# Kernel optimization log

Hardware: AMD Instinct MI355X
Metric: run time of the kernel (lower is better)

Reference implementation:

```python
import jax, jax.numpy as jnp
import numpy as np

N_ATOMS = 100000
N_PAIRS = 3200000
N_PROP = 16
N_BASIS = 10
W = 16  # MLP width for pp/pi/ii nodes


def setup_inputs() -> dict:
    key = jax.random.key(0)
    ks = jax.random.split(key, 16)
    s = 0.1
    inp = {
        "ind_2": jax.random.randint(ks[0], (N_PAIRS, 2), 0, N_ATOMS),
        "p1": jax.random.normal(ks[1], (N_ATOMS, N_PROP), dtype=jnp.float32),
        "basis": jax.random.normal(ks[2], (N_PAIRS, N_BASIS), dtype=jnp.float32),
        # pp_pre: [16,16], bias=True
        "Wpre0": jax.random.normal(ks[3], (N_PROP, W), dtype=jnp.float32) * s,
        "bpre0": jnp.zeros((W,), dtype=jnp.float32),
        "Wpre1": jax.random.normal(ks[4], (W, W), dtype=jnp.float32) * s,
        "bpre1": jnp.zeros((W,), dtype=jnp.float32),
        # pi: input 2*W -> W -> W*n_basis, bias=True
        "Wpi0": jax.random.normal(ks[5], (2 * W, W), dtype=jnp.float32) * s,
        "bpi0": jnp.zeros((W,), dtype=jnp.float32),
        "Wpi1": jax.random.normal(ks[6], (W, W * N_BASIS), dtype=jnp.float32) * s,
        "bpi1": jnp.zeros((W * N_BASIS,), dtype=jnp.float32),
        # ii: [16,16], bias=False
        "Wii0": jax.random.normal(ks[7], (W, W), dtype=jnp.float32) * s,
        "Wii1": jax.random.normal(ks[8], (W, W), dtype=jnp.float32) * s,
        # pp_post: [16,16], bias=False
        "Wpost0": jax.random.normal(ks[9], (W, W), dtype=jnp.float32) * s,
        "Wpost1": jax.random.normal(ks[10], (W, W), dtype=jnp.float32) * s,
    }
    return inp


def reference(ind_2, p1, basis, Wpre0, bpre0, Wpre1, bpre1,
              Wpi0, bpi0, Wpi1, bpi1, Wii0, Wii1, Wpost0, Wpost1):
    act = jnp.tanh
    n_atoms = p1.shape[0]
    # pp_pre: per-atom FF (activation on every dense, bias=True)
    p1_in = act(p1 @ Wpre0 + bpre0)
    p1_in = act(p1_in @ Wpre1 + bpre1)
    # PI: gather pair endpoints, concat, MLP, contract with radial basis
    h = jnp.concatenate([p1_in[ind_2[:, 0]], p1_in[ind_2[:, 1]]], axis=-1)  # (P, 2W)
    h = act(h @ Wpi0 + bpi0)                                                # (P, W)
    h = act(h @ Wpi1 + bpi1)                                                # (P, W*n_basis)
    h = h.reshape(h.shape[0], -1, basis.shape[-1])                          # (P, W, n_basis)
    i_pair = jnp.einsum('pcb,pb->pc', h, basis)                             # (P, W)
    # II: pair-mixing FF (bias=False)
    i_pair = act(i_pair @ Wii0)
    i_pair = act(i_pair @ Wii1)
    # IP: scatter-sum pair features back to atoms at ind_2[:,0]
    p_sum = jax.ops.segment_sum(i_pair, ind_2[:, 0], num_segments=n_atoms)  # (A, W)
    # pp_post (bias=False)
    p1_new = act(p_sum @ Wpost0)
    p1_new = act(p1_new @ Wpost1)
    return (p1_new, i_pair)
```

## Files before the change

kernel.cpp:

```cpp
#include <hip/hip_runtime.h>

#define N_ATOMS 100000
#define N_PAIRS 3200000
#define N_PROP 16
#define N_BASIS 10
#define W 16
#define NSUP (N_PAIRS / 32)
#define SCAN_BLK 1024
#define NB ((N_ATOMS + SCAN_BLK - 1) / SCAN_BLK)
#define SC 2.88539008177792681f

typedef short  s16x8  __attribute__((ext_vector_type(8)));
typedef float  f32x4  __attribute__((ext_vector_type(4)));
typedef float  f32x16 __attribute__((ext_vector_type(16)));

__device__ __forceinline__ float tanh_pre(float y) {
    float e = __builtin_amdgcn_exp2f(y);
    return 1.0f - 2.0f * __builtin_amdgcn_rcpf(e + 1.0f);
}
__device__ __forceinline__ float fast_tanh(float x) {
    float e = __builtin_amdgcn_exp2f(x * SC);
    return 1.0f - 2.0f * __builtin_amdgcn_rcpf(e + 1.0f);
}
__device__ __forceinline__ unsigned short bf16r(float f) {
    union { float f; unsigned u; } v; v.f = f;
    unsigned r = v.u + 0x7FFFu + ((v.u >> 16) & 1u);
    return (unsigned short)(r >> 16);
}
__device__ __forceinline__ unsigned cvt_pk_bf16(float a, float b) {
    unsigned r;
    asm("v_cvt_pk_bf16_f32 %0, %1, %2" : "=v"(r) : "v"(a), "v"(b));
    return r;
}
__device__ __forceinline__ float bitf(unsigned u) {
    union { unsigned u; float f; } v; v.u = u; return v.f;
}

__global__ __launch_bounds__(256) void k_pp_pre(
    const float* __restrict__ p1,
    const float* __restrict__ W0, const float* __restrict__ b0,
    const float* __restrict__ W1, const float* __restrict__ b1,
    const float* __restrict__ Wpi0, const float* __restrict__ bpi0,
    float* __restrict__ ytop, float* __restrict__ ybot)
{
    int a = blockIdx.x * 256 + threadIdx.x;
    if (a >= N_ATOMS) return;
    const float4* src = reinterpret_cast<const float4*>(p1 + (size_t)a * N_PROP);
    float4 v0 = src[0], v1 = src[1], v2 = src[2], v3 = src[3];
    float x[N_PROP] = {v0.x,v0.y,v0.z,v0.w, v1.x,v1.y,v1.z,v1.w,
                       v2.x,v2.y,v2.z,v2.w, v3.x,v3.y,v3.z,v3.w};
    float h[W];
#pragma unroll
    for (int c = 0; c < W; ++c) h[c] = b0[c];
#pragma unroll
    for (int k = 0; k < N_PROP; ++k)
#pragma unroll
        for (int c = 0; c < W; ++c) h[c] += x[k] * W0[k*W + c];
#pragma unroll
    for (int c = 0; c < W; ++c) h[c] = fast_tanh(h[c]);
    float y[W];
#pragma unroll
    for (int c = 0; c < W; ++c) y[c] = b1[c];
#pragma unroll
    for (int k = 0; k < W; ++k)
#pragma unroll
        for (int c = 0; c < W; ++c) y[c] += h[k] * W1[k*W + c];
    float t[W];
#pragma unroll
    for (int c = 0; c < W; ++c) t[c] = fast_tanh(y[c]);

    float yt[W], yb[W];
#pragma unroll
    for (int c = 0; c < W; ++c) { yt[c] = bpi0[c]; yb[c] = 0.0f; }
#pragma unroll
    for (int k = 0; k < W; ++k)
#pragma unroll
        for (int c = 0; c < W; ++c) {
            yt[c] += t[k] * Wpi0[k*W + c];
            yb[c] += t[k] * Wpi0[(W + k)*W + c];
        }
    float4* dt = reinterpret_cast<float4*>(ytop + (size_t)a * W);
    float4* db = reinterpret_cast<float4*>(ybot + (size_t)a * W);
#pragma unroll
    for (int q = 0; q < 4; ++q) {
        dt[q] = make_float4(SC*yt[4*q], SC*yt[4*q+1], SC*yt[4*q+2], SC*yt[4*q+3]);
        db[q] = make_float4(SC*yb[4*q], SC*yb[4*q+1], SC*yb[4*q+2], SC*yb[4*q+3]);
    }
}

template<int USE_RANK>
__global__ __launch_bounds__(256) void k_pair_mfma(
    const int*   __restrict__ ind2,
    const float* __restrict__ basis,
    const float* __restrict__ ytop,
    const float* __restrict__ ybot,
    const float* __restrict__ Wpi1, const float* __restrict__ bpi1,
    const float* __restrict__ Wii0, const float* __restrict__ Wii1,
    float* __restrict__ i_pair_out,
    const unsigned* __restrict__ starts,
    const unsigned* __restrict__ rank,
    unsigned* __restrict__ cursor,
    float* __restrict__ svals)
{
    __shared__ s16x8 aw_lds[5][2][32];
    __shared__ s16x8 ab_lds[5][2][32];

    const int lane = threadIdx.x & 63;
    const int wv   = threadIdx.x >> 6;
    const int col  = lane & 31;
    const int h    = lane >> 5;

    for (int e = threadIdx.x; e < 320; e += 256) {
        int T = e >> 6, hh = (e >> 5) & 1, row = e & 31;
        int colW = (4*(row >> 3) + (row & 3)) * N_BASIS + 2*T + ((row >> 2) & 1);
        s16x8 wfrag, bfrag;
#pragma unroll
        for (int j = 0; j < 8; ++j) {
            int k = 8*hh + j;
            wfrag[j] = (short)bf16r(SC * Wpi1[k*(W*N_BASIS) + colW]);
            bfrag[j] = (short)((k == 0) ? bf16r(SC * bpi1[colW]) : 0);
        }
        aw_lds[T][hh][row] = wfrag;
        ab_lds[T][hh][row] = bfrag;
    }

    s16x8 a3, a4;
#pragma unroll
    for (int j = 0; j < 8; ++j) {
        int k = 8*h + j;
        a3[j] = (short)(col < W ? bf16r(SC * Wii0[k*W + col]) : 0);
        a4[j] = (short)(col < W ? bf16r(SC * Wii1[k*W + col]) : 0);
    }
    s16x8 Bones = {0,0,0,0,0,0,0,0};
    if (h == 0) Bones[0] = (short)0x3F80;

    __syncthreads();

    const int stride = gridDim.x * 4;
    int sup = blockIdx.x * 4 + wv;
    if (sup >= NSUP) return;
    const int2* ind2v = reinterpret_cast<const int2*>(ind2);

    int2 ij = ind2v[(size_t)sup * 32 + col];
    f32x4 yt0 = *reinterpret_cast<const f32x4*>(ytop + (size_t)ij.x * W + 8*h);
    f32x4 yt1 = *reinterpret_cast<const f32x4*>(ytop + (size_t)ij.x * W + 8*h + 4);
    f32x4 yb0 = *reinterpret_cast<const f32x4*>(ybot + (size_t)ij.y * W + 8*h);
    f32x4 yb1 = *reinterpret_cast<const f32x4*>(ybot + (size_t)ij.y * W + 8*h + 4);

    for (; sup < NSUP; sup += stride) {
        const int p0 = sup * 32;
        const int p  = p0 + col;
        const int nsup = (sup + stride < NSUP) ? (sup + stride) : sup;

        int2 nij = ind2v[(size_t)nsup * 32 + col];

        float h0[8];
#pragma unroll
        for (int j = 0; j < 4; ++j) h0[j]     = tanh_pre(yt0[j] + yb0[j]);
#pragma unroll
        for (int j = 0; j < 4; ++j) h0[4 + j] = tanh_pre(yt1[j] + yb1[j]);
        unsigned w0h = cvt_pk_bf16(h0[0], h0[1]);
        unsigned w1h = cvt_pk_bf16(h0[2], h0[3]);
        unsigned w2h = cvt_pk_bf16(h0[4], h0[5]);
        unsigned w3h = cvt_pk_bf16(h0[6], h0[7]);
        unsigned w0l = cvt_pk_bf16(h0[0] - bitf(w0h << 16), h0[1] - bitf(w0h & 0xFFFF0000u));
        unsigned w1l = cvt_pk_bf16(h0[2] - bitf(w1h << 16), h0[3] - bitf(w1h & 0xFFFF0000u));
        unsigned w2l = cvt_pk_bf16(h0[4] - bitf(w2h << 16), h0[5] - bitf(w2h & 0xFFFF0000u));
        unsigned w3l = cvt_pk_bf16(h0[6] - bitf(w3h << 16), h0[7] - bitf(w3h & 0xFFFF0000u));
        union { unsigned u[4]; s16x8 v; } BH, BL;
        BH.u[0] = w0h; BH.u[1] = w1h; BH.u[2] = w2h; BH.u[3] = w3h;
        BL.u[0] = w0l; BL.u[1] = w1l; BL.u[2] = w2l; BL.u[3] = w3l;
        s16x8 B2h = BH.v, B2l = BL.v;

        const float2* bb = reinterpret_cast<const float2*>(basis + (size_t)p * N_BASIS);
        float bsel[5];
#pragma unroll
        for (int q = 0; q < 5; ++q) {
            float2 t2 = bb[q];
            bsel[q] = h ? t2.y : t2.x;
        }

        float v[16];
#pragma unroll
        for (int i = 0; i < 16; ++i) v[i] = 0.0f;
#pragma unroll
        for (int T = 0; T < 5; ++T) {
            s16x8 af = aw_lds[T][h][col];
            s16x8 ab = ab_lds[T][h][col];
            f32x16 z = {0.0f};
            z = __builtin_amdgcn_mfma_f32_32x32x16_bf16(ab, Bones, z, 0, 0, 0);
            z = __builtin_amdgcn_mfma_f32_32x32x16_bf16(af, B2h,  z, 0, 0, 0);
            z = __builtin_amdgcn_mfma_f32_32x32x16_bf16(af, B2l,  z, 0, 0, 0);
#pragma unroll
            for (int i = 0; i < 16; ++i)
                v[i] += tanh_pre(z[i]) * bsel[T];
        }

        f32x4 nyt0 = *reinterpret_cast<const f32x4*>(ytop + (size_t)nij.x * W + 8*h);
        f32x4 nyt1 = *reinterpret_cast<const f32x4*>(ytop + (size_t)nij.x * W + 8*h + 4);
        f32x4 nyb0 = *reinterpret_cast<const f32x4*>(ybot + (size_t)nij.y * W + 8*h);
        f32x4 nyb1 = *reinterpret_cast<const f32x4*>(ybot + (size_t)nij.y * W + 8*h + 4);

        float own[8], snd[8];
        if (h == 0) {
#pragma unroll
            for (int j = 0; j < 8; ++j) { own[j] = v[j]; snd[j] = v[8 + j]; }
        } else {
#pragma unroll
            for (int j = 0; j < 8; ++j) { own[j] = v[8 + j]; snd[j] = v[j]; }
        }
        float vf[8];
#pragma unroll
        for (int j = 0; j < 8; ++j) vf[j] = own[j] + __shfl_xor(snd[j], 32);

        union { unsigned u[4]; s16x8 v; } B3u;
        B3u.u[0] = cvt_pk_bf16(vf[0], vf[1]);
        B3u.u[1] = cvt_pk_bf16(vf[2], vf[3]);
        B3u.u[2] = cvt_pk_bf16(vf[4], vf[5]);
        B3u.u[3] = cvt_pk_bf16(vf[6], vf[7]);
        f32x16 ua = {0.0f};
        ua = __builtin_amdgcn_mfma_f32_32x32x16_bf16(a3, B3u.v, ua, 0, 0, 0);
        float u[8];
#pragma unroll
        for (int i = 0; i < 8; ++i) u[i] = tanh_pre(ua[i]);

        float uo[4], us[4];
        if (h == 0) {
#pragma unroll
            for (int j = 0; j < 4; ++j) { uo[j] = u[j]; us[j] = u[4 + j]; }
        } else {
#pragma unroll
            for (int j = 0; j < 4; ++j) { uo[j] = u[4 + j]; us[j] = u[j]; }
        }
        float ur[4];
#pragma unroll
        for (int j = 0; j < 4; ++j) ur[j] = __shfl_xor(us[j], 32);
        union { unsigned u[4]; s16x8 v; } B4u;
        if (h == 0) {
            B4u.u[0] = cvt_pk_bf16(uo[0], uo[1]);
            B4u.u[1] = cvt_pk_bf16(uo[2], uo[3]);
            B4u.u[2] = cvt_pk_bf16(ur[0], ur[1]);
            B4u.u[3] = cvt_pk_bf16(ur[2], ur[3]);
        } else {
            B4u.u[0] = cvt_pk_bf16(ur[0], ur[1]);
            B4u.u[1] = cvt_pk_bf16(ur[2], ur[3]);
            B4u.u[2] = cvt_pk_bf16(uo[0], uo[1]);
            B4u.u[3] = cvt_pk_bf16(uo[2], uo[3]);
        }
        f32x16 wa = {0.0f};
        wa = __builtin_amdgcn_mfma_f32_32x32x16_bf16(a4, B4u.v, wa, 0, 0, 0);
        float wq[8];
#pragma unroll
        for (int i = 0; i < 8; ++i) wq[i] = tanh_pre(wa[i]);

        unsigned pos;
        if (USE_RANK) {
            pos = starts[ij.x] + rank[p];
        } else {
            unsigned pp = 0;
            if (h == 0) pp = atomicAdd(&cursor[ij.x], 1u);
            pos = (unsigned)__shfl((int)pp, col);
        }

        const int rk0 = lane & 15;
        const int q   = lane >> 4;
#pragma unroll
        for (int k = 0; k < 2; ++k) {
            int row = 16*k + rk0;
            int src = row + 32*(q & 1);
            float vA0 = __shfl(wq[0], src), vA1 = __shfl(wq[1], src);
            float vA2 = __shfl(wq[2], src), vA3 = __shfl(wq[3], src);
            float vB0 = __shfl(wq[4], src), vB1 = __shfl(wq[5], src);
            float vB2 = __shfl(wq[6], src), vB3 = __shfl(wq[7], src);
            bool hiq = (q >= 2);
            f32x4 val = { hiq ? vB0 : vA0, hiq ? vB1 : vA1,
                          hiq ? vB2 : vA2, hiq ? vB3 : vA3 };
            unsigned posr = (unsigned)__shfl((int)pos, row);
            __builtin_nontemporal_store(val,
                reinterpret_cast<f32x4*>(i_pair_out + (size_t)(p0 + row) * W + q*4));
            __builtin_nontemporal_store(val,
                reinterpret_cast<f32x4*>(svals + (size_t)posr * W + q*4));
        }

        ij = nij;
        yt0 = nyt0; yt1 = nyt1; yb0 = nyb0; yb1 = nyb1;
    }
}

__global__ __launch_bounds__(256) void k_count(const int* __restrict__ ind2,
                                               unsigned* __restrict__ counts,
                                               unsigned* __restrict__ rank)
{
    int t = blockIdx.x * 256 + threadIdx.x;
    if (t >= N_PAIRS / 2) return;
    int4 ii = reinterpret_cast<const int4*>(ind2)[t];
    unsigned r0 = atomicAdd(&counts[ii.x], 1u);
    unsigned r1 = atomicAdd(&counts[ii.z], 1u);
    uint2 rr; rr.x = r0; rr.y = r1;
    *reinterpret_cast<uint2*>(rank + 2*t) = rr;
}

__global__ __launch_bounds__(SCAN_BLK) void k_scanA(const unsigned* __restrict__ counts,
                                                    unsigned* __restrict__ starts,
                                                    unsigned* __restrict__ bsum)
{
    __shared__ unsigned sc[SCAN_BLK];
    int a = blockIdx.x * SCAN_BLK + threadIdx.x;
    unsigned c = (a < N_ATOMS) ? counts[a] : 0u;
    sc[threadIdx.x] = c;
    __syncthreads();
    for (int off = 1; off < SCAN_BLK; off <<= 1) {
        unsigned v = sc[threadIdx.x];
        unsigned add = (threadIdx.x >= off) ? sc[threadIdx.x - off] : 0u;
        __syncthreads();
        sc[threadIdx.x] = v + add;
        __syncthreads();
    }
    if (a < N_ATOMS) starts[a] = sc[threadIdx.x] - c;
    if (threadIdx.x == SCAN_BLK - 1) bsum[blockIdx.x] = sc[SCAN_BLK - 1];
}

__global__ __launch_bounds__(128) void k_scanB(const unsigned* __restrict__ bsum,
                                               unsigned* __restrict__ boff)
{
    __shared__ unsigned s[128];
    int t = threadIdx.x;
    unsigned v = (t < NB) ? bsum[t] : 0u;
    s[t] = v;
    __syncthreads();
    for (int off = 1; off < 128; off <<= 1) {
        unsigned x = s[t];
        unsigned add = (t >= off) ? s[t - off] : 0u;
        __syncthreads();
        s[t] = x + add;
        __syncthreads();
    }
    if (t < NB) boff[t] = s[t] - v;
}

__global__ __launch_bounds__(SCAN_BLK) void k_scanC(unsigned* __restrict__ starts,
                                                    const unsigned* __restrict__ boff,
                                                    unsigned* __restrict__ cursor)
{
    int a = blockIdx.x * SCAN_BLK + threadIdx.x;
    if (a >= N_ATOMS) return;
    unsigned s = starts[a] + boff[blockIdx.x];
    starts[a] = s;
    cursor[a] = s;
}

__global__ __launch_bounds__(256) void k_reduce_stream(const unsigned* __restrict__ starts,
                                                       const unsigned* __restrict__ counts,
                                                       const float* __restrict__ svals,
                                                       float* __restrict__ p_sum)
{
    int a = blockIdx.x * 4 + (threadIdx.x >> 6);
    if (a >= N_ATOMS) return;
    int lane = threadIdx.x & 63;
    int c4 = lane & 3;
    int q  = lane >> 2;
    unsigned n = counts[a], st = starts[a];
    f32x4 acc = {0.f, 0.f, 0.f, 0.f};
    for (unsigned k = q; k < n; k += 16)
        acc += *reinterpret_cast<const f32x4*>(svals + (size_t)(st + k) * W + c4*4);
#pragma unroll
    for (int off = 4; off < 64; off <<= 1) {
        acc[0] += __shfl_xor(acc[0], off);
        acc[1] += __shfl_xor(acc[1], off);
        acc[2] += __shfl_xor(acc[2], off);
        acc[3] += __shfl_xor(acc[3], off);
    }
    if (lane < 4)
        *reinterpret_cast<f32x4*>(p_sum + (size_t)a * W + lane*4) = acc;
}

__global__ __launch_bounds__(256) void k_pp_post(
    const float* __restrict__ p_sum,
    const float* __restrict__ W0, const float* __restrict__ W1,
    float* __restrict__ p1_new)
{
    int a = blockIdx.x * 256 + threadIdx.x;
    if (a >= N_ATOMS) return;
    const float4* src = reinterpret_cast<const float4*>(p_sum + (size_t)a * W);
    float4 v0 = src[0], v1 = src[1], v2 = src[2], v3 = src[3];
    float x[W] = {v0.x,v0.y,v0.z,v0.w, v1.x,v1.y,v1.z,v1.w,
                  v2.x,v2.y,v2.z,v2.w, v3.x,v3.y,v3.z,v3.w};
    float h[W];
#pragma unroll
    for (int c = 0; c < W; ++c) h[c] = 0.0f;
#pragma unroll
    for (int k = 0; k < W; ++k)
#pragma unroll
        for (int c = 0; c < W; ++c) h[c] += x[k] * W0[k*W + c];
#pragma unroll
    for (int c = 0; c < W; ++c) h[c] = fast_tanh(h[c]);
    float y[W];
#pragma unroll
    for (int c = 0; c < W; ++c) y[c] = 0.0f;
#pragma unroll
    for (int k = 0; k < W; ++k)
#pragma unroll
        for (int c = 0; c < W; ++c) y[c] += h[k] * W1[k*W + c];
    float4* dst = reinterpret_cast<float4*>(p1_new + (size_t)a * W);
    dst[0] = make_float4(fast_tanh(y[0]),  fast_tanh(y[1]),  fast_tanh(y[2]),  fast_tanh(y[3]));
    dst[1] = make_float4(fast_tanh(y[4]),  fast_tanh(y[5]),  fast_tanh(y[6]),  fast_tanh(y[7]));
    dst[2] = make_float4(fast_tanh(y[8]),  fast_tanh(y[9]),  fast_tanh(y[10]), fast_tanh(y[11]));
    dst[3] = make_float4(fast_tanh(y[12]), fast_tanh(y[13]), fast_tanh(y[14]), fast_tanh(y[15]));
}

extern "C" void kernel_launch(void* const* d_in, const int* in_sizes, int n_in,
                              void* d_out, int out_size, void* d_ws, size_t ws_size,
                              hipStream_t stream) {
    const int*   ind2   = (const int*)d_in[0];
    const float* p1     = (const float*)d_in[1];
    const float* basis  = (const float*)d_in[2];
    const float* Wpre0  = (const float*)d_in[3];
    const float* bpre0  = (const float*)d_in[4];
    const float* Wpre1  = (const float*)d_in[5];
    const float* bpre1  = (const float*)d_in[6];
    const float* Wpi0   = (const float*)d_in[7];
    const float* bpi0   = (const float*)d_in[8];
    const float* Wpi1   = (const float*)d_in[9];
    const float* bpi1   = (const float*)d_in[10];
    const float* Wii0   = (const float*)d_in[11];
    const float* Wii1   = (const float*)d_in[12];
    const float* Wpost0 = (const float*)d_in[13];
    const float* Wpost1 = (const float*)d_in[14];

    float* out    = (float*)d_out;
    float* p1_new = out;
    float* i_pair = out + (size_t)N_ATOMS * W;

    char* ws = (char*)d_ws;
    float*    ytop   = (float*)ws;                                ws += (size_t)N_ATOMS * W * 4;
    float*    ybot   = (float*)ws;                                ws += (size_t)N_ATOMS * W * 4;
    float*    p_sum  = (float*)ws;                                ws += (size_t)N_ATOMS * W * 4;
    unsigned* counts = (unsigned*)ws;                             ws += (size_t)N_ATOMS * 4;
    unsigned* starts = (unsigned*)ws;                             ws += (size_t)N_ATOMS * 4;
    unsigned* cursor = (unsigned*)ws;                             ws += (size_t)N_ATOMS * 4;
    unsigned* bsum   = (unsigned*)ws;                             ws += 1024 * 4;
    unsigned* boff   = (unsigned*)ws;                             ws += 1024 * 4;
    float*    svals  = (float*)ws;                                ws += (size_t)N_PAIRS * W * 4;
    unsigned* rank   = (unsigned*)ws;                             ws += (size_t)N_PAIRS * 4;

    int use_rank = (ws_size >= (size_t)(ws - (char*)d_ws));

    hipMemsetAsync(counts, 0, (size_t)N_ATOMS * sizeof(unsigned), stream);
    k_pp_pre<<<(N_ATOMS + 255) / 256, 256, 0, stream>>>(p1, Wpre0, bpre0, Wpre1, bpre1,
                                                        Wpi0, bpi0, ytop, ybot);
    k_count<<<(N_PAIRS / 2 + 255) / 256, 256, 0, stream>>>(ind2, counts, use_rank ? rank : cursor);
    k_scanA<<<NB, SCAN_BLK, 0, stream>>>(counts, starts, bsum);
    k_scanB<<<1, 128, 0, stream>>>(bsum, boff);
    k_scanC<<<NB, SCAN_BLK, 0, stream>>>(starts, boff, cursor);

    if (use_rank) {
        k_pair_mfma<1><<<2560, 256, 0, stream>>>(ind2, basis, ytop, ybot,
                                                 Wpi1, bpi1, Wii0, Wii1,
                                                 i_pair, starts, rank, cursor, svals);
    } else {
        k_pair_mfma<0><<<2560, 256, 0, stream>>>(ind2, basis, ytop, ybot,
                                                 Wpi1, bpi1, Wii0, Wii1,
                                                 i_pair, starts, rank, cursor, svals);
    }
    k_reduce_stream<<<(N_ATOMS + 3) / 4, 256, 0, stream>>>(starts, counts, svals, p_sum);
    k_pp_post<<<(N_ATOMS + 255) / 256, 256, 0, stream>>>(p_sum, Wpost0, Wpost1, p1_new);
}
```

Baseline: 484.7 us.

## Replace sorted pair-value copy with index-based gather in segment reduction

The pair kernel no longer writes a second, atom-sorted copy of every pair feature vector. Instead a new kernel builds a sorted pair-index array from the counting ranks, and the reduction gathers rows of the i_pair output through that index. The intent is to drop a full extra write and read of the pair features, at the cost of random-access reads in the reduction. The block-offset scan is also folded into the final scan kernel, and the atomic-cursor fallback is removed.

```diff
diff --git a/kernel.cpp b/kernel.cpp
--- a/kernel.cpp
+++ b/kernel.cpp
@@ -88,7 +88,6 @@
     }
 }
 
-template<int USE_RANK>
 __global__ __launch_bounds__(256) void k_pair_mfma(
     const int*   __restrict__ ind2,
     const float* __restrict__ basis,
@@ -96,11 +95,7 @@
     const float* __restrict__ ybot,
     const float* __restrict__ Wpi1, const float* __restrict__ bpi1,
     const float* __restrict__ Wii0, const float* __restrict__ Wii1,
-    float* __restrict__ i_pair_out,
-    const unsigned* __restrict__ starts,
-    const unsigned* __restrict__ rank,
-    unsigned* __restrict__ cursor,
-    float* __restrict__ svals)
+    float* __restrict__ i_pair_out)
 {
     __shared__ s16x8 aw_lds[5][2][32];
     __shared__ s16x8 ab_lds[5][2][32];
@@ -253,15 +248,6 @@
 #pragma unroll
         for (int i = 0; i < 8; ++i) wq[i] = tanh_pre(wa[i]);
 
-        unsigned pos;
-        if (USE_RANK) {
-            pos = starts[ij.x] + rank[p];
-        } else {
-            unsigned pp = 0;
-            if (h == 0) pp = atomicAdd(&cursor[ij.x], 1u);
-            pos = (unsigned)__shfl((int)pp, col);
-        }
-
         const int rk0 = lane & 15;
         const int q   = lane >> 4;
 #pragma unroll
@@ -275,11 +261,8 @@
             bool hiq = (q >= 2);
             f32x4 val = { hiq ? vB0 : vA0, hiq ? vB1 : vA1,
                           hiq ? vB2 : vA2, hiq ? vB3 : vA3 };
-            unsigned posr = (unsigned)__shfl((int)pos, row);
             __builtin_nontemporal_store(val,
                 reinterpret_cast<f32x4*>(i_pair_out + (size_t)(p0 + row) * W + q*4));
-            __builtin_nontemporal_store(val,
-                reinterpret_cast<f32x4*>(svals + (size_t)posr * W + q*4));
         }
 
         ij = nij;
@@ -320,38 +303,42 @@
     if (threadIdx.x == SCAN_BLK - 1) bsum[blockIdx.x] = sc[SCAN_BLK - 1];
 }
 
-__global__ __launch_bounds__(128) void k_scanB(const unsigned* __restrict__ bsum,
-                                               unsigned* __restrict__ boff)
+__global__ __launch_bounds__(SCAN_BLK) void k_scanC(unsigned* __restrict__ starts,
+                                                    const unsigned* __restrict__ bsum)
 {
     __shared__ unsigned s[128];
-    int t = threadIdx.x;
-    unsigned v = (t < NB) ? bsum[t] : 0u;
-    s[t] = v;
+    if (threadIdx.x < 128)
+        s[threadIdx.x] = (threadIdx.x < NB) ? bsum[threadIdx.x] : 0u;
     __syncthreads();
     for (int off = 1; off < 128; off <<= 1) {
-        unsigned x = s[t];
-        unsigned add = (t >= off) ? s[t - off] : 0u;
+        unsigned x = (threadIdx.x < 128) ? s[threadIdx.x] : 0u;
+        unsigned add = (threadIdx.x >= off && threadIdx.x < 128) ? s[threadIdx.x - off] : 0u;
         __syncthreads();
-        s[t] = x + add;
+        if (threadIdx.x < 128) s[threadIdx.x] = x + add;
         __syncthreads();
     }
-    if (t < NB) boff[t] = s[t] - v;
-}
-
-__global__ __launch_bounds__(SCAN_BLK) void k_scanC(unsigned* __restrict__ starts,
-                                                    const unsigned* __restrict__ boff,
-                                                    unsigned* __restrict__ cursor)
-{
+    unsigned boffb = (blockIdx.x == 0) ? 0u : s[blockIdx.x - 1];
     int a = blockIdx.x * SCAN_BLK + threadIdx.x;
-    if (a >= N_ATOMS) return;
-    unsigned s = starts[a] + boff[blockIdx.x];
-    starts[a] = s;
-    cursor[a] = s;
-}
-
-__global__ __launch_bounds__(256) void k_reduce_stream(const unsigned* __restrict__ starts,
+    if (a < N_ATOMS) starts[a] += boffb;
+}
+
+__global__ __launch_bounds__(256) void k_sidx(const int* __restrict__ ind2,
+                                              const unsigned* __restrict__ rank,
+                                              const unsigned* __restrict__ starts,
+                                              unsigned* __restrict__ sidx)
+{
+    int t = blockIdx.x * 256 + threadIdx.x;
+    if (t >= N_PAIRS / 2) return;
+    int4 ii = reinterpret_cast<const int4*>(ind2)[t];
+    uint2 rr = *reinterpret_cast<const uint2*>(rank + 2*t);
+    sidx[starts[ii.x] + rr.x] = (unsigned)(2*t);
+    sidx[starts[ii.z] + rr.y] = (unsigned)(2*t + 1);
+}
+
+__global__ __launch_bounds__(256) void k_reduce_gather(const unsigned* __restrict__ starts,
                                                        const unsigned* __restrict__ counts,
-                                                       const float* __restrict__ svals,
+                                                       const unsigned* __restrict__ sidx,
+                                                       const float* __restrict__ i_pair,
                                                        float* __restrict__ p_sum)
 {
     int a = blockIdx.x * 4 + (threadIdx.x >> 6);
@@ -361,8 +348,10 @@
     int q  = lane >> 2;
     unsigned n = counts[a], st = starts[a];
     f32x4 acc = {0.f, 0.f, 0.f, 0.f};
-    for (unsigned k = q; k < n; k += 16)
-        acc += *reinterpret_cast<const f32x4*>(svals + (size_t)(st + k) * W + c4*4);
+    for (unsigned k = q; k < n; k += 16) {
+        unsigned pid = sidx[st + k];
+        acc += *reinterpret_cast<const f32x4*>(i_pair + (size_t)pid * W + c4*4);
+    }
 #pragma unroll
     for (int off = 4; off < 64; off <<= 1) {
         acc[0] += __shfl_xor(acc[0], off);
@@ -437,31 +426,20 @@
     float*    p_sum  = (float*)ws;                                ws += (size_t)N_ATOMS * W * 4;
     unsigned* counts = (unsigned*)ws;                             ws += (size_t)N_ATOMS * 4;
     unsigned* starts = (unsigned*)ws;                             ws += (size_t)N_ATOMS * 4;
-    unsigned* cursor = (unsigned*)ws;                             ws += (size_t)N_ATOMS * 4;
     unsigned* bsum   = (unsigned*)ws;                             ws += 1024 * 4;
-    unsigned* boff   = (unsigned*)ws;                             ws += 1024 * 4;
-    float*    svals  = (float*)ws;                                ws += (size_t)N_PAIRS * W * 4;
     unsigned* rank   = (unsigned*)ws;                             ws += (size_t)N_PAIRS * 4;
-
-    int use_rank = (ws_size >= (size_t)(ws - (char*)d_ws));
+    unsigned* sidx   = (unsigned*)ws;                             ws += (size_t)N_PAIRS * 4;
 
     hipMemsetAsync(counts, 0, (size_t)N_ATOMS * sizeof(unsigned), stream);
     k_pp_pre<<<(N_ATOMS + 255) / 256, 256, 0, stream>>>(p1, Wpre0, bpre0, Wpre1, bpre1,
                                                         Wpi0, bpi0, ytop, ybot);
-    k_count<<<(N_PAIRS / 2 + 255) / 256, 256, 0, stream>>>(ind2, counts, use_rank ? rank : cursor);
+    k_count<<<(N_PAIRS / 2 + 255) / 256, 256, 0, stream>>>(ind2, counts, rank);
     k_scanA<<<NB, SCAN_BLK, 0, stream>>>(counts, starts, bsum);
-    k_scanB<<<1, 128, 0, stream>>>(bsum, boff);
-    k_scanC<<<NB, SCAN_BLK, 0, stream>>>(starts, boff, cursor);
-
-    if (use_rank) {
-        k_pair_mfma<1><<<2560, 256, 0, stream>>>(ind2, basis, ytop, ybot,
-                                                 Wpi1, bpi1, Wii0, Wii1,
-                                                 i_pair, starts, rank, cursor, svals);
-    } else {
-        k_pair_mfma<0><<<2560, 256, 0, stream>>>(ind2, basis, ytop, ybot,
-                                                 Wpi1, bpi1, Wii0, Wii1,
-                                                 i_pair, starts, rank, cursor, svals);
-    }
-    k_reduce_stream<<<(N_ATOMS + 3) / 4, 256, 0, stream>>>(starts, counts, svals, p_sum);
+    k_scanC<<<NB, SCAN_BLK, 0, stream>>>(starts, bsum);
+    k_sidx<<<(N_PAIRS / 2 + 255) / 256, 256, 0, stream>>>(ind2, rank, starts, sidx);
+
+    k_pair_mfma<<<2560, 256, 0, stream>>>(ind2, basis, ytop, ybot,
+                                          Wpi1, bpi1, Wii0, Wii1, i_pair);
+    k_reduce_gather<<<(N_ATOMS + 3) / 4, 256, 0, stream>>>(starts, counts, sidx, i_pair, p_sum);
     k_pp_post<<<(N_ATOMS + 255) / 256, 256, 0, stream>>>(p_sum, Wpost0, Wpost1, p1_new);
 }
```

Result: no change. 486.5 us (+0.4%).
